# Kernel optimization log

Measured on AMD Instinct MI355X. Metric: run time of the kernel, lower is better.

## Reference

```python
import jax, jax.numpy as jnp
import numpy as np

N = 100000       # nodes
E = 3200000      # edges (avg degree 32)
IN = 64          # in_channels
HID = 32         # hidden_channels
HEADS = 2
OUT = 1
EPS = 1e-5       # LayerNorm eps
SLOPE = 0.2      # LeakyReLU negative slope (PyG default)


def setup_inputs() -> dict:
    key = jax.random.key(0)
    ks = jax.random.split(key, 18)
    def nrm(k, shape, scale=0.1):
        return jax.random.normal(k, shape, dtype=jnp.float32) * scale
    return {
        "x": jax.random.normal(ks[0], (N, IN), dtype=jnp.float32),
        "edge_index": jax.random.randint(ks[1], (2, E), 0, N, dtype=jnp.int64),
        # GATConv layer 1 (concat=True)
        "W1": nrm(ks[2], (IN, HEADS * HID)),
        "a_src1": nrm(ks[3], (HEADS, HID)),
        "a_dst1": nrm(ks[4], (HEADS, HID)),
        "b1": jnp.zeros((HEADS * HID,), jnp.float32),
        "ln1_g": jnp.ones((HEADS * HID,), jnp.float32),
        "ln1_b": jnp.zeros((HEADS * HID,), jnp.float32),
        # GATConv layer 2 (heads=1, concat=False)
        "W2": nrm(ks[5], (HEADS * HID, HID)),
        "a_src2": nrm(ks[6], (1, HID)),
        "a_dst2": nrm(ks[7], (1, HID)),
        "b2": jnp.zeros((HID,), jnp.float32),
        "ln2_g": jnp.ones((HID,), jnp.float32),
        "ln2_b": jnp.zeros((HID,), jnp.float32),
        # output Linear
        "Wout": nrm(ks[8], (HID, OUT)),
        "bout": jnp.zeros((OUT,), jnp.float32),
    }


def layer_norm(x, g, b):
    mu = jnp.mean(x, axis=-1, keepdims=True)
    var = jnp.mean(jnp.square(x - mu), axis=-1, keepdims=True)
    return (x - mu) * jax.lax.rsqrt(var + EPS) * g + b


def gat_conv(x, edge_index, W, a_src, a_dst, bias, heads, ch, concat):
    """PyG GATConv (add_self_loops=True, bias=True), eval mode (no dropout)."""
    n = x.shape[0]
    loop = jnp.arange(n, dtype=edge_index.dtype)
    src = jnp.concatenate([edge_index[0], loop])   # [E+N]
    dst = jnp.concatenate([edge_index[1], loop])   # [E+N]
    h = (x @ W).reshape(n, heads, ch)              # [N,H,C]
    al_src = jnp.sum(h * a_src, axis=-1)           # [N,H]
    al_dst = jnp.sum(h * a_dst, axis=-1)           # [N,H]
    logits = jax.nn.leaky_relu(al_src[src] + al_dst[dst], SLOPE)  # [E+N,H]
    # segment softmax over destination nodes
    m = jax.lax.stop_gradient(jax.ops.segment_max(logits, dst, num_segments=n))
    e = jnp.exp(logits - m[dst])
    denom = jax.ops.segment_sum(e, dst, num_segments=n)
    alpha = e / denom[dst]                         # [E+N,H]
    out = jax.ops.segment_sum(h[src] * alpha[:, :, None], dst, num_segments=n)  # [N,H,C]
    out = out.reshape(n, heads * ch) if concat else out.mean(axis=1)
    return out + bias


def reference(x, edge_index, W1, a_src1, a_dst1, b1, ln1_g, ln1_b,
              W2, a_src2, a_dst2, b2, ln2_g, ln2_b, Wout, bout):
    h = gat_conv(x, edge_index, W1, a_src1, a_dst1, b1, HEADS, HID, True)
    h = jax.nn.elu(layer_norm(h, ln1_g, ln1_b))
    h = gat_conv(h, edge_index, W2, a_src2, a_dst2, b2, 1, HID, False)
    h = jax.nn.elu(layer_norm(h, ln2_g, ln2_b))
    return h @ Wout + bout  # [N, OUT]
```

## Files before the change

kernel.cpp:

```cpp
#include <hip/hip_runtime.h>

#define EPS 1e-5f
#define SLOPE 0.2f
#define MAXK 512
#define SEGCAP 12288
#define PBATCH 16384

__device__ __forceinline__ float leaky(float z) {
    return fmaxf(z, 0.f) + SLOPE * fminf(z, 0.f);
}
__device__ __forceinline__ ushort f2bf(float f) {
    unsigned u = __float_as_uint(f);
    u += 0x7FFFu + ((u >> 16) & 1u);
    return (ushort)(u >> 16);
}
__device__ __forceinline__ float bf2f(ushort b) {
    return __uint_as_float(((unsigned)b) << 16);
}

__global__ __launch_bounds__(256) void hist0(
    const int* __restrict__ ei, int E, int K, int* __restrict__ ghist) {
    __shared__ int h[MAXK];
    int t = threadIdx.x;
    for (int i = t; i < K; i += 256) h[i] = 0;
    __syncthreads();
    int base = blockIdx.x * PBATCH;
    for (int j = 0; j < PBATCH / 256; j++) {
        int e = base + j * 256 + t;
        if (e < E) atomicAdd(&h[ei[E + e] >> 8], 1);
    }
    __syncthreads();
    for (int i = t; i < K; i += 256) if (h[i]) atomicAdd(&ghist[i], h[i]);
}

__global__ __launch_bounds__(512) void scanK(
    const int* __restrict__ ghist, int K, int* __restrict__ segbase,
    int* __restrict__ cursor) {
    __shared__ int sc[512];
    int t = threadIdx.x;
    int v = (t < K) ? ghist[t] : 0;
    sc[t] = v;
    __syncthreads();
    for (int off = 1; off < 512; off <<= 1) {
        int x = (t >= off) ? sc[t - off] : 0;
        __syncthreads();
        sc[t] += x;
        __syncthreads();
    }
    if (t < K) { int ex = sc[t] - v; segbase[t] = ex; cursor[t] = ex; }
    if (t == K - 1) segbase[K] = sc[t];
}

__global__ __launch_bounds__(256) void part1(
    const int* __restrict__ ei, int E, int K, int* __restrict__ cursor,
    unsigned* __restrict__ part) {
    __shared__ int h[MAXK];
    __shared__ int gp[MAXK];
    __shared__ int run[MAXK];
    int t = threadIdx.x;
    for (int i = t; i < K; i += 256) { h[i] = 0; run[i] = 0; }
    __syncthreads();
    int base = blockIdx.x * PBATCH;
    for (int j = 0; j < PBATCH / 256; j++) {
        int e = base + j * 256 + t;
        if (e < E) atomicAdd(&h[ei[E + e] >> 8], 1);
    }
    __syncthreads();
    for (int i = t; i < K; i += 256)
        gp[i] = h[i] ? atomicAdd(&cursor[i], h[i]) : 0;
    __syncthreads();
    for (int j = 0; j < PBATCH / 256; j++) {
        int e = base + j * 256 + t;
        if (e < E) {
            int s = ei[e], d = ei[E + e];
            int b = d >> 8;
            int p = atomicAdd(&run[b], 1);
            part[gp[b] + p] = ((unsigned)s << 8) | (unsigned)(d & 255);
        }
    }
}

__global__ __launch_bounds__(256) void sortseg(
    const int* __restrict__ segbase, int N,
    unsigned* __restrict__ part, int* __restrict__ nodeofs, int* __restrict__ cnt,
    int* __restrict__ perm) {
    __shared__ int h2[2048];
    __shared__ int sc[256];
    __shared__ int ex[256];
    __shared__ unsigned outb[SEGCAP];
    int b = blockIdx.x, t = threadIdx.x;
    int base = segbase[b];
    int sz = segbase[b + 1] - base;
    if (sz > SEGCAP) sz = SEGCAP;
    for (int i = t; i < 2048; i += 256) h2[i] = 0;
    __syncthreads();
    for (int i = t; i < sz; i += 256) {
        unsigned code = part[base + i];
        int key = ((code & 255) << 3) | ((code >> 22) & 7);
        atomicAdd(&h2[key], 1);
    }
    __syncthreads();
    int loc[8];
    int v = 0;
#pragma unroll
    for (int i = 0; i < 8; i++) { loc[i] = h2[t * 8 + i]; v += loc[i]; }
    sc[t] = v;
    __syncthreads();
    for (int off = 1; off < 256; off <<= 1) {
        int x = (t >= off) ? sc[t - off] : 0;
        __syncthreads();
        sc[t] += x;
        __syncthreads();
    }
    int exv = sc[t] - v;
    {
        int run = exv;
#pragma unroll
        for (int i = 0; i < 8; i++) { h2[t * 8 + i] = run; run += loc[i]; }
    }
    int n = b * 256 + t;
    if (n < N) { cnt[n] = v; nodeofs[n] = base + exv; }
    __syncthreads();
    for (int i = t; i < sz; i += 256) {
        unsigned code = part[base + i];
        int key = ((code & 255) << 3) | ((code >> 22) & 7);
        int p = atomicAdd(&h2[key], 1);
        outb[p] = code >> 8;
    }
    __syncthreads();
    for (int i = t; i < sz; i += 256) part[base + i] = outb[i];
    __syncthreads();
    h2[t] = 0;
    __syncthreads();
    int dbin = min(v, 255);
    if (n < N) atomicAdd(&h2[dbin], 1);
    __syncthreads();
    int hv = h2[t];
    sc[t] = hv;
    __syncthreads();
    for (int off = 1; off < 256; off <<= 1) {
        int x = (t >= off) ? sc[t - off] : 0;
        __syncthreads();
        sc[t] += x;
        __syncthreads();
    }
    ex[t] = sc[t] - hv;
    __syncthreads();
    if (n < N) {
        int r = atomicAdd(&ex[dbin], 1);
        perm[b * 256 + r] = n;
    }
}

__global__ __launch_bounds__(256) void prep1(
    const float* __restrict__ x, const float* __restrict__ W1,
    const float* __restrict__ as1, const float* __restrict__ ad1,
    ushort* __restrict__ h1b, float* __restrict__ al_s, float* __restrict__ al_d, int N) {
    __shared__ float Ws[64 * 64];
    __shared__ float xs[16][68];
    int t = threadIdx.x;
    for (int i = t; i < 64 * 64; i += 256) Ws[i] = W1[i];
    int base = blockIdx.x * 16;
    for (int i = t; i < 256; i += 256) {
        int rr = i >> 4, kk = i & 15;
        int gr = base + rr;
        float4 vx = (gr < N) ? ((const float4*)x)[(size_t)gr * 16 + kk]
                             : make_float4(0.f, 0.f, 0.f, 0.f);
        *(float4*)&xs[rr][kk * 4] = vx;
    }
    __syncthreads();
    int wv = t >> 6, c = t & 63;
    int r0 = base + wv * 4;
    float acc0 = 0.f, acc1 = 0.f, acc2 = 0.f, acc3 = 0.f;
#pragma unroll
    for (int k = 0; k < 64; k += 4) {
        float4 x0 = *(const float4*)&xs[wv * 4 + 0][k];
        float4 x1 = *(const float4*)&xs[wv * 4 + 1][k];
        float4 x2 = *(const float4*)&xs[wv * 4 + 2][k];
        float4 x3 = *(const float4*)&xs[wv * 4 + 3][k];
        float w0 = Ws[(k + 0) * 64 + c];
        float w1 = Ws[(k + 1) * 64 + c];
        float w2 = Ws[(k + 2) * 64 + c];
        float w3 = Ws[(k + 3) * 64 + c];
        acc0 = fmaf(x0.x, w0, acc0); acc1 = fmaf(x1.x, w0, acc1);
        acc2 = fmaf(x2.x, w0, acc2); acc3 = fmaf(x3.x, w0, acc3);
        acc0 = fmaf(x0.y, w1, acc0); acc1 = fmaf(x1.y, w1, acc1);
        acc2 = fmaf(x2.y, w1, acc2); acc3 = fmaf(x3.y, w1, acc3);
        acc0 = fmaf(x0.z, w2, acc0); acc1 = fmaf(x1.z, w2, acc1);
        acc2 = fmaf(x2.z, w2, acc2); acc3 = fmaf(x3.z, w2, acc3);
        acc0 = fmaf(x0.w, w3, acc0); acc1 = fmaf(x1.w, w3, acc1);
        acc2 = fmaf(x2.w, w3, acc2); acc3 = fmaf(x3.w, w3, acc3);
    }
    int head = c >> 5, cc = c & 31;
    float asc = as1[head * 32 + cc], adc = ad1[head * 32 + cc];
    float vs0 = acc0 * asc, vd0 = acc0 * adc;
    float vs1 = acc1 * asc, vd1 = acc1 * adc;
    float vs2 = acc2 * asc, vd2 = acc2 * adc;
    float vs3 = acc3 * asc, vd3 = acc3 * adc;
#pragma unroll
    for (int off = 1; off < 32; off <<= 1) {
        vs0 += __shfl_xor(vs0, off); vd0 += __shfl_xor(vd0, off);
        vs1 += __shfl_xor(vs1, off); vd1 += __shfl_xor(vd1, off);
        vs2 += __shfl_xor(vs2, off); vd2 += __shfl_xor(vd2, off);
        vs3 += __shfl_xor(vs3, off); vd3 += __shfl_xor(vd3, off);
    }
    if (r0 + 0 < N) h1b[(size_t)(r0 + 0) * 64 + c] = f2bf(acc0);
    if (r0 + 1 < N) h1b[(size_t)(r0 + 1) * 64 + c] = f2bf(acc1);
    if (r0 + 2 < N) h1b[(size_t)(r0 + 2) * 64 + c] = f2bf(acc2);
    if (r0 + 3 < N) h1b[(size_t)(r0 + 3) * 64 + c] = f2bf(acc3);
    if (cc == 0) {
        if (r0 + 0 < N) { al_s[(r0 + 0) * 2 + head] = vs0; al_d[(r0 + 0) * 2 + head] = vd0; }
        if (r0 + 1 < N) { al_s[(r0 + 1) * 2 + head] = vs1; al_d[(r0 + 1) * 2 + head] = vd1; }
        if (r0 + 2 < N) { al_s[(r0 + 2) * 2 + head] = vs2; al_d[(r0 + 2) * 2 + head] = vd2; }
        if (r0 + 3 < N) { al_s[(r0 + 3) * 2 + head] = vs3; al_d[(r0 + 3) * 2 + head] = vd3; }
    }
}

__global__ __launch_bounds__(256) void aggB1(
    const ushort* __restrict__ h1b, const float* __restrict__ als,
    const float* __restrict__ ald, const int* __restrict__ nodeofs,
    const int* __restrict__ cnt, const unsigned* __restrict__ csr,
    const int* __restrict__ perm,
    const float* __restrict__ b1, const float* __restrict__ g1,
    const float* __restrict__ bb1, ushort* __restrict__ h1out, int N) {
    int lane = threadIdx.x & 63;
    int grp = lane >> 4, q = lane & 15;
    int gbase = grp << 4;
    int idx = blockIdx.x * 16 + (threadIdx.x >> 6) * 4 + grp;
    bool valid = idx < N;
    int nc = perm[min(idx, N - 1)];
    int head = q >> 3;
    const float2* als2 = (const float2*)als;
    const float2* ald2 = (const float2*)ald;
    float2 adv = ald2[nc], asv = als2[nc];
    float ad0 = adv.x, ad1v = adv.y;
    float wsf = __expf(leaky((head ? asv.y : asv.x) + (head ? ad1v : ad0)));
    const ushort4* h4 = (const ushort4*)h1b;
    ushort4 hs = h4[(unsigned)nc * 16 + q];
    float a0 = wsf * bf2f(hs.x), a1 = wsf * bf2f(hs.y);
    float a2 = wsf * bf2f(hs.z), a3 = wsf * bf2f(hs.w);
    float l0p = 0.f, l1p = 0.f;
    int ofs = valid ? nodeofs[nc] : 0;
    int deg = valid ? cnt[nc] : 0;
    int degm1 = max(deg - 1, 0);
    int degmax = deg;
    degmax = max(degmax, __shfl_xor(degmax, 16));
    degmax = max(degmax, __shfl_xor(degmax, 32));
    for (int eb = 0; eb < degmax; eb += 16) {
        int j = ofs + min(eb + q, degm1);
        int sq = min((int)csr[j], N - 1);
        float2 av = als2[sq];
        float z0 = leaky(av.x + ad0);
        float z1 = leaky(av.y + ad1v);
        bool ev = (eb + q < deg);
        float w0q = ev ? __expf(z0) : 0.f;
        float w1q = ev ? __expf(z1) : 0.f;
        l0p += w0q;
        l1p += w1q;
#pragma unroll
        for (int jj = 0; jj < 16; jj++) {
            int s = __shfl(sq, gbase + jj);
            float w0 = __shfl(w0q, gbase + jj);
            float w1 = __shfl(w1q, gbase + jj);
            float w = head ? w1 : w0;
            ushort4 hv = h4[(unsigned)s * 16 + q];
            a0 = fmaf(w, bf2f(hv.x), a0);
            a1 = fmaf(w, bf2f(hv.y), a1);
            a2 = fmaf(w, bf2f(hv.z), a2);
            a3 = fmaf(w, bf2f(hv.w), a3);
        }
    }
#pragma unroll
    for (int off = 1; off < 16; off <<= 1) {
        l0p += __shfl_xor(l0p, off);
        l1p += __shfl_xor(l1p, off);
    }
    if (!valid) return;
    float l = (head ? l1p : l0p) + wsf;
    float inv = 1.f / l;
    float4 bv = ((const float4*)b1)[q];
    float v0 = a0 * inv + bv.x, v1 = a1 * inv + bv.y;
    float v2 = a2 * inv + bv.z, v3 = a3 * inv + bv.w;
    float s1 = v0 + v1 + v2 + v3;
#pragma unroll
    for (int off = 1; off < 16; off <<= 1) s1 += __shfl_xor(s1, off);
    float mu = s1 * (1.f / 64.f);
    float d0 = v0 - mu, d1 = v1 - mu, d2 = v2 - mu, d3 = v3 - mu;
    float s2v = d0 * d0 + d1 * d1 + d2 * d2 + d3 * d3;
#pragma unroll
    for (int off = 1; off < 16; off <<= 1) s2v += __shfl_xor(s2v, off);
    float rs = rsqrtf(s2v * (1.f / 64.f) + EPS);
    float4 gv = ((const float4*)g1)[q];
    float4 bbv = ((const float4*)bb1)[q];
    float y0 = d0 * rs * gv.x + bbv.x;
    float y1 = d1 * rs * gv.y + bbv.y;
    float y2 = d2 * rs * gv.z + bbv.z;
    float y3 = d3 * rs * gv.w + bbv.w;
    y0 = (y0 > 0.f) ? y0 : (__expf(y0) - 1.f);
    y1 = (y1 > 0.f) ? y1 : (__expf(y1) - 1.f);
    y2 = (y2 > 0.f) ? y2 : (__expf(y2) - 1.f);
    y3 = (y3 > 0.f) ? y3 : (__expf(y3) - 1.f);
    ((ushort4*)h1out)[(unsigned)nc * 16 + q] =
        make_ushort4(f2bf(y0), f2bf(y1), f2bf(y2), f2bf(y3));
}

__global__ __launch_bounds__(256) void prep2(
    const ushort* __restrict__ h1ob, const float* __restrict__ W2,
    const float* __restrict__ as2, const float* __restrict__ ad2,
    ushort* __restrict__ h2b, float* __restrict__ al_s, float* __restrict__ al_d, int N) {
    __shared__ float Ws[64 * 32];
    __shared__ float xs[32][68];
    int t = threadIdx.x;
    for (int i = t; i < 64 * 32; i += 256) Ws[i] = W2[i];
    int base = blockIdx.x * 32;
    const ushort4* hv4 = (const ushort4*)h1ob;
    for (int i = t; i < 512; i += 256) {
        int rr = i >> 4, kk = i & 15;
        int gr = base + rr;
        ushort4 u = (gr < N) ? hv4[(unsigned)gr * 16 + kk] : make_ushort4(0, 0, 0, 0);
        xs[rr][kk * 4 + 0] = bf2f(u.x);
        xs[rr][kk * 4 + 1] = bf2f(u.y);
        xs[rr][kk * 4 + 2] = bf2f(u.z);
        xs[rr][kk * 4 + 3] = bf2f(u.w);
    }
    __syncthreads();
    int wv = t >> 6;
    int lane = t & 63;
    int half = lane >> 5, c = lane & 31;
    int rbase = wv * 8 + half * 4;
    int r0 = base + rbase;
    float acc0 = 0.f, acc1 = 0.f, acc2 = 0.f, acc3 = 0.f;
#pragma unroll
    for (int k = 0; k < 64; k += 4) {
        float4 x0 = *(const float4*)&xs[rbase + 0][k];
        float4 x1 = *(const float4*)&xs[rbase + 1][k];
        float4 x2 = *(const float4*)&xs[rbase + 2][k];
        float4 x3 = *(const float4*)&xs[rbase + 3][k];
        float w0 = Ws[(k + 0) * 32 + c];
        float w1 = Ws[(k + 1) * 32 + c];
        float w2 = Ws[(k + 2) * 32 + c];
        float w3 = Ws[(k + 3) * 32 + c];
        acc0 = fmaf(x0.x, w0, acc0); acc1 = fmaf(x1.x, w0, acc1);
        acc2 = fmaf(x2.x, w0, acc2); acc3 = fmaf(x3.x, w0, acc3);
        acc0 = fmaf(x0.y, w1, acc0); acc1 = fmaf(x1.y, w1, acc1);
        acc2 = fmaf(x2.y, w1, acc2); acc3 = fmaf(x3.y, w1, acc3);
        acc0 = fmaf(x0.z, w2, acc0); acc1 = fmaf(x1.z, w2, acc1);
        acc2 = fmaf(x2.z, w2, acc2); acc3 = fmaf(x3.z, w2, acc3);
        acc0 = fmaf(x0.w, w3, acc0); acc1 = fmaf(x1.w, w3, acc1);
        acc2 = fmaf(x2.w, w3, acc2); acc3 = fmaf(x3.w, w3, acc3);
    }
    float asc = as2[c], adc = ad2[c];
    float vs0 = acc0 * asc, vd0 = acc0 * adc;
    float vs1 = acc1 * asc, vd1 = acc1 * adc;
    float vs2 = acc2 * asc, vd2 = acc2 * adc;
    float vs3 = acc3 * asc, vd3 = acc3 * adc;
#pragma unroll
    for (int off = 1; off < 32; off <<= 1) {
        vs0 += __shfl_xor(vs0, off); vd0 += __shfl_xor(vd0, off);
        vs1 += __shfl_xor(vs1, off); vd1 += __shfl_xor(vd1, off);
        vs2 += __shfl_xor(vs2, off); vd2 += __shfl_xor(vd2, off);
        vs3 += __shfl_xor(vs3, off); vd3 += __shfl_xor(vd3, off);
    }
    if (r0 + 0 < N) h2b[(size_t)(r0 + 0) * 32 + c] = f2bf(acc0);
    if (r0 + 1 < N) h2b[(size_t)(r0 + 1) * 32 + c] = f2bf(acc1);
    if (r0 + 2 < N) h2b[(size_t)(r0 + 2) * 32 + c] = f2bf(acc2);
    if (r0 + 3 < N) h2b[(size_t)(r0 + 3) * 32 + c] = f2bf(acc3);
    if (c == 0) {
        if (r0 + 0 < N) { al_s[r0 + 0] = vs0; al_d[r0 + 0] = vd0; }
        if (r0 + 1 < N) { al_s[r0 + 1] = vs1; al_d[r0 + 1] = vd1; }
        if (r0 + 2 < N) { al_s[r0 + 2] = vs2; al_d[r0 + 2] = vd2; }
        if (r0 + 3 < N) { al_s[r0 + 3] = vs3; al_d[r0 + 3] = vd3; }
    }
}

__global__ __launch_bounds__(256) void aggB2(
    const ushort* __restrict__ h2b, const float* __restrict__ als,
    const float* __restrict__ ald, const int* __restrict__ nodeofs,
    const int* __restrict__ cnt, const unsigned* __restrict__ csr,
    const int* __restrict__ perm,
    const float* __restrict__ b2, const float* __restrict__ g2,
    const float* __restrict__ bb2, const float* __restrict__ Wout,
    const float* __restrict__ bout, float* __restrict__ out, int N) {
    int lane = threadIdx.x & 63;
    int grp = lane >> 3, q = lane & 7;
    int gbase = grp << 3;
    int idx = blockIdx.x * 32 + (threadIdx.x >> 6) * 8 + grp;
    bool valid = idx < N;
    int nc = perm[min(idx, N - 1)];
    float myad = ald[nc];
    float wsf = __expf(leaky(als[nc] + myad));
    const ushort4* h4 = (const ushort4*)h2b;
    ushort4 hs = h4[(unsigned)nc * 8 + q];
    float a0 = wsf * bf2f(hs.x), a1 = wsf * bf2f(hs.y);
    float a2 = wsf * bf2f(hs.z), a3 = wsf * bf2f(hs.w);
    float lp = 0.f;
    int ofs = valid ? nodeofs[nc] : 0;
    int deg = valid ? cnt[nc] : 0;
    int degm1 = max(deg - 1, 0);
    int degmax = deg;
    degmax = max(degmax, __shfl_xor(degmax, 8));
    degmax = max(degmax, __shfl_xor(degmax, 16));
    degmax = max(degmax, __shfl_xor(degmax, 32));
    for (int eb = 0; eb < degmax; eb += 8) {
        int j = ofs + min(eb + q, degm1);
        int sq = min((int)csr[j], N - 1);
        float z = leaky(als[sq] + myad);
        float wq = (eb + q < deg) ? __expf(z) : 0.f;
        lp += wq;
#pragma unroll
        for (int jj = 0; jj < 8; jj++) {
            int s = __shfl(sq, gbase + jj);
            float w = __shfl(wq, gbase + jj);
            ushort4 hv = h4[(unsigned)s * 8 + q];
            a0 = fmaf(w, bf2f(hv.x), a0);
            a1 = fmaf(w, bf2f(hv.y), a1);
            a2 = fmaf(w, bf2f(hv.z), a2);
            a3 = fmaf(w, bf2f(hv.w), a3);
        }
    }
#pragma unroll
    for (int off = 1; off < 8; off <<= 1) lp += __shfl_xor(lp, off);
    if (!valid) return;
    float l = lp + wsf;
    float inv = 1.f / l;
    float4 bv = ((const float4*)b2)[q];
    float v0 = a0 * inv + bv.x, v1 = a1 * inv + bv.y;
    float v2 = a2 * inv + bv.z, v3 = a3 * inv + bv.w;
    float s1 = v0 + v1 + v2 + v3;
#pragma unroll
    for (int off = 1; off < 8; off <<= 1) s1 += __shfl_xor(s1, off);
    float mu = s1 * (1.f / 32.f);
    float d0 = v0 - mu, d1 = v1 - mu, d2 = v2 - mu, d3 = v3 - mu;
    float s2v = d0 * d0 + d1 * d1 + d2 * d2 + d3 * d3;
#pragma unroll
    for (int off = 1; off < 8; off <<= 1) s2v += __shfl_xor(s2v, off);
    float rs = rsqrtf(s2v * (1.f / 32.f) + EPS);
    float4 gv = ((const float4*)g2)[q];
    float4 bbv = ((const float4*)bb2)[q];
    float y0 = d0 * rs * gv.x + bbv.x;
    float y1 = d1 * rs * gv.y + bbv.y;
    float y2 = d2 * rs * gv.z + bbv.z;
    float y3 = d3 * rs * gv.w + bbv.w;
    y0 = (y0 > 0.f) ? y0 : (__expf(y0) - 1.f);
    y1 = (y1 > 0.f) ? y1 : (__expf(y1) - 1.f);
    y2 = (y2 > 0.f) ? y2 : (__expf(y2) - 1.f);
    y3 = (y3 > 0.f) ? y3 : (__expf(y3) - 1.f);
    float4 wo = ((const float4*)Wout)[q];
    float p = y0 * wo.x + y1 * wo.y + y2 * wo.z + y3 * wo.w;
#pragma unroll
    for (int off = 1; off < 8; off <<= 1) p += __shfl_xor(p, off);
    if (q == 0) out[nc] = p + bout[0];
}

extern "C" void kernel_launch(void* const* d_in, const int* in_sizes, int n_in,
                              void* d_out, int out_size, void* d_ws, size_t ws_size,
                              hipStream_t stream) {
    const float* x    = (const float*)d_in[0];
    const int*   ei   = (const int*)d_in[1];
    const float* W1   = (const float*)d_in[2];
    const float* as1  = (const float*)d_in[3];
    const float* ad1  = (const float*)d_in[4];
    const float* b1   = (const float*)d_in[5];
    const float* g1   = (const float*)d_in[6];
    const float* bb1  = (const float*)d_in[7];
    const float* W2   = (const float*)d_in[8];
    const float* as2  = (const float*)d_in[9];
    const float* ad2  = (const float*)d_in[10];
    const float* b2   = (const float*)d_in[11];
    const float* g2   = (const float*)d_in[12];
    const float* bb2  = (const float*)d_in[13];
    const float* Wout = (const float*)d_in[14];
    const float* bout = (const float*)d_in[15];
    float* out = (float*)d_out;

    const int N = in_sizes[0] / 64;
    const int E = in_sizes[1] / 2;
    const int K = (N + 255) / 256;

    auto align_up = [](size_t v) { return (v + 255) & ~(size_t)255; };
    char* ws = (char*)d_ws;
    unsigned* part    = (unsigned*)ws; ws += align_up((size_t)E * 4);
    int*      nodeofs = (int*)ws;      ws += align_up((size_t)N * 4);
    int*      cnt     = (int*)ws;      ws += align_up((size_t)N * 4);
    int*      perm    = (int*)ws;      ws += align_up((size_t)(K * 256) * 4);
    int*      ghist   = (int*)ws;      ws += align_up((size_t)(MAXK) * 4);
    int*      segbase = (int*)ws;      ws += align_up((size_t)(MAXK + 1) * 4);
    int*      cursor  = (int*)ws;      ws += align_up((size_t)(MAXK) * 4);
    ushort*   h1b     = (ushort*)ws;   ws += align_up((size_t)N * 64 * 2);
    ushort*   h1ob    = (ushort*)ws;   ws += align_up((size_t)N * 64 * 2);
    ushort*   h2b     = (ushort*)ws;   ws += align_up((size_t)N * 32 * 2);
    float*    al1s    = (float*)ws;    ws += align_up((size_t)N * 2 * 4);
    float*    al1d    = (float*)ws;    ws += align_up((size_t)N * 2 * 4);
    float*    al2s    = (float*)ws;    ws += align_up((size_t)N * 4);
    float*    al2d    = (float*)ws;    ws += align_up((size_t)N * 4);

    const int EB = (E + PBATCH - 1) / PBATCH;

    hipMemsetAsync(ghist, 0, (size_t)K * 4, stream);
    hist0<<<EB, 256, 0, stream>>>(ei, E, K, ghist);
    scanK<<<1, 512, 0, stream>>>(ghist, K, segbase, cursor);
    part1<<<EB, 256, 0, stream>>>(ei, E, K, cursor, part);
    sortseg<<<K, 256, 0, stream>>>(segbase, N, part, nodeofs, cnt, perm);

    prep1<<<(N + 15) / 16, 256, 0, stream>>>(x, W1, as1, ad1, h1b, al1s, al1d, N);
    aggB1<<<(N + 15) / 16, 256, 0, stream>>>(h1b, al1s, al1d, nodeofs, cnt, part,
                                             perm, b1, g1, bb1, h1ob, N);
    prep2<<<(N + 31) / 32, 256, 0, stream>>>(h1ob, W2, as2, ad2, h2b, al2s, al2d, N);
    aggB2<<<(N + 31) / 32, 256, 0, stream>>>(h2b, al2s, al2d, nodeofs, cnt, part,
                                             perm, b2, g2, bb2, Wout, bout, out, N);
}
```

Before: 363.8 us.

## Use fixed-capacity segments to drop histogram pass and pad CSR rows for vector loads

Replaces the global histogram and scan kernels with fixed-capacity per-segment buckets (SEGCAP each), so the edge partition runs as one pass that uses atomic counters per segment. sortseg now pads each node's adjacency list to a multiple of 4 with zeros and sorts on a finer key. The aggregation kernels read neighbor indices with int4 vector loads instead of broadcasting them through shuffles. In layer 1 the two head weights are packed into one bf16 pair so each edge needs a single shuffle. This removes two kernel launches and a full read of the edge list, and cuts shuffle traffic. In exchange, the partition buffer is larger, bf16 rounding is applied to the attention weights, and edges beyond SEGCAP in a segment are silently dropped. The int4 loads can also read past the padded row into the next node's entries, which is only safe because their weights are zero.

```diff
diff --git a/kernel.cpp b/kernel.cpp
--- a/kernel.cpp
+++ b/kernel.cpp
@@ -18,41 +18,8 @@
     return __uint_as_float(((unsigned)b) << 16);
 }
 
-__global__ __launch_bounds__(256) void hist0(
-    const int* __restrict__ ei, int E, int K, int* __restrict__ ghist) {
-    __shared__ int h[MAXK];
-    int t = threadIdx.x;
-    for (int i = t; i < K; i += 256) h[i] = 0;
-    __syncthreads();
-    int base = blockIdx.x * PBATCH;
-    for (int j = 0; j < PBATCH / 256; j++) {
-        int e = base + j * 256 + t;
-        if (e < E) atomicAdd(&h[ei[E + e] >> 8], 1);
-    }
-    __syncthreads();
-    for (int i = t; i < K; i += 256) if (h[i]) atomicAdd(&ghist[i], h[i]);
-}
-
-__global__ __launch_bounds__(512) void scanK(
-    const int* __restrict__ ghist, int K, int* __restrict__ segbase,
-    int* __restrict__ cursor) {
-    __shared__ int sc[512];
-    int t = threadIdx.x;
-    int v = (t < K) ? ghist[t] : 0;
-    sc[t] = v;
-    __syncthreads();
-    for (int off = 1; off < 512; off <<= 1) {
-        int x = (t >= off) ? sc[t - off] : 0;
-        __syncthreads();
-        sc[t] += x;
-        __syncthreads();
-    }
-    if (t < K) { int ex = sc[t] - v; segbase[t] = ex; cursor[t] = ex; }
-    if (t == K - 1) segbase[K] = sc[t];
-}
-
 __global__ __launch_bounds__(256) void part1(
-    const int* __restrict__ ei, int E, int K, int* __restrict__ cursor,
+    const int* __restrict__ ei, int E, int K, int* __restrict__ segcnt,
     unsigned* __restrict__ part) {
     __shared__ int h[MAXK];
     __shared__ int gp[MAXK];
@@ -67,44 +34,45 @@
     }
     __syncthreads();
     for (int i = t; i < K; i += 256)
-        gp[i] = h[i] ? atomicAdd(&cursor[i], h[i]) : 0;
+        gp[i] = h[i] ? atomicAdd(&segcnt[i], h[i]) : 0;
     __syncthreads();
     for (int j = 0; j < PBATCH / 256; j++) {
         int e = base + j * 256 + t;
         if (e < E) {
             int s = ei[e], d = ei[E + e];
             int b = d >> 8;
-            int p = atomicAdd(&run[b], 1);
-            part[gp[b] + p] = ((unsigned)s << 8) | (unsigned)(d & 255);
+            int p = atomicAdd(&run[b], 1) + gp[b];
+            if (p < SEGCAP)
+                part[(size_t)b * SEGCAP + p] = ((unsigned)s << 8) | (unsigned)(d & 255);
         }
     }
 }
 
 __global__ __launch_bounds__(256) void sortseg(
-    const int* __restrict__ segbase, int N,
+    const int* __restrict__ segcnt, int N,
     unsigned* __restrict__ part, int* __restrict__ nodeofs, int* __restrict__ cnt,
     int* __restrict__ perm) {
-    __shared__ int h2[2048];
+    __shared__ int h2[4096];
     __shared__ int sc[256];
     __shared__ int ex[256];
     __shared__ unsigned outb[SEGCAP];
     int b = blockIdx.x, t = threadIdx.x;
-    int base = segbase[b];
-    int sz = segbase[b + 1] - base;
-    if (sz > SEGCAP) sz = SEGCAP;
-    for (int i = t; i < 2048; i += 256) h2[i] = 0;
+    size_t base = (size_t)b * SEGCAP;
+    int sz = min(segcnt[b], SEGCAP);
+    for (int i = t; i < 4096; i += 256) h2[i] = 0;
     __syncthreads();
     for (int i = t; i < sz; i += 256) {
         unsigned code = part[base + i];
-        int key = ((code & 255) << 3) | ((code >> 22) & 7);
+        int key = ((code & 255) << 4) | ((code >> 21) & 15);
         atomicAdd(&h2[key], 1);
     }
     __syncthreads();
-    int loc[8];
+    int loc[16];
     int v = 0;
 #pragma unroll
-    for (int i = 0; i < 8; i++) { loc[i] = h2[t * 8 + i]; v += loc[i]; }
-    sc[t] = v;
+    for (int i = 0; i < 16; i++) { loc[i] = h2[t * 16 + i]; v += loc[i]; }
+    int vp = (v + 3) & ~3;
+    sc[t] = vp;
     __syncthreads();
     for (int off = 1; off < 256; off <<= 1) {
         int x = (t >= off) ? sc[t - off] : 0;
@@ -112,23 +80,26 @@
         sc[t] += x;
         __syncthreads();
     }
-    int exv = sc[t] - v;
+    int exv = sc[t] - vp;
     {
         int run = exv;
 #pragma unroll
-        for (int i = 0; i < 8; i++) { h2[t * 8 + i] = run; run += loc[i]; }
+        for (int i = 0; i < 16; i++) { h2[t * 16 + i] = run; run += loc[i]; }
     }
     int n = b * 256 + t;
-    if (n < N) { cnt[n] = v; nodeofs[n] = base + exv; }
+    if (n < N) { cnt[n] = v; nodeofs[n] = (int)(base + exv); }
+    int szp = sc[255];
+    __syncthreads();
+    for (int i = t; i < szp; i += 256) outb[i] = 0;
     __syncthreads();
     for (int i = t; i < sz; i += 256) {
         unsigned code = part[base + i];
-        int key = ((code & 255) << 3) | ((code >> 22) & 7);
+        int key = ((code & 255) << 4) | ((code >> 21) & 15);
         int p = atomicAdd(&h2[key], 1);
         outb[p] = code >> 8;
     }
     __syncthreads();
-    for (int i = t; i < sz; i += 256) part[base + i] = outb[i];
+    for (int i = t; i < szp; i += 256) part[base + i] = outb[i];
     __syncthreads();
     h2[t] = 0;
     __syncthreads();
@@ -230,6 +201,7 @@
     bool valid = idx < N;
     int nc = perm[min(idx, N - 1)];
     int head = q >> 3;
+    int hshift = head << 4;
     const float2* als2 = (const float2*)als;
     const float2* ald2 = (const float2*)ald;
     float2 adv = ald2[nc], asv = als2[nc];
@@ -246,9 +218,10 @@
     int degmax = deg;
     degmax = max(degmax, __shfl_xor(degmax, 16));
     degmax = max(degmax, __shfl_xor(degmax, 32));
+    unsigned nm1 = (unsigned)(N - 1);
     for (int eb = 0; eb < degmax; eb += 16) {
         int j = ofs + min(eb + q, degm1);
-        int sq = min((int)csr[j], N - 1);
+        int sq = (int)min((unsigned)csr[j], nm1);
         float2 av = als2[sq];
         float z0 = leaky(av.x + ad0);
         float z1 = leaky(av.y + ad1v);
@@ -257,12 +230,16 @@
         float w1q = ev ? __expf(z1) : 0.f;
         l0p += w0q;
         l1p += w1q;
+        unsigned wp = ((unsigned)f2bf(w1q) << 16) | f2bf(w0q);
+        const int4* c4 = (const int4*)(csr + ofs + eb);
+        int4 ca = c4[0], cb = c4[1], cc4 = c4[2], cd = c4[3];
+        int ss[16] = {ca.x, ca.y, ca.z, ca.w, cb.x, cb.y, cb.z, cb.w,
+                      cc4.x, cc4.y, cc4.z, cc4.w, cd.x, cd.y, cd.z, cd.w};
 #pragma unroll
         for (int jj = 0; jj < 16; jj++) {
-            int s = __shfl(sq, gbase + jj);
-            float w0 = __shfl(w0q, gbase + jj);
-            float w1 = __shfl(w1q, gbase + jj);
-            float w = head ? w1 : w0;
+            int s = (int)min((unsigned)ss[jj], nm1);
+            unsigned wpj = (unsigned)__shfl((int)wp, gbase + jj);
+            float w = bf2f((ushort)((wpj >> hshift) & 0xFFFFu));
             ushort4 hv = h4[(unsigned)s * 16 + q];
             a0 = fmaf(w, bf2f(hv.x), a0);
             a1 = fmaf(w, bf2f(hv.y), a1);
@@ -401,15 +378,19 @@
     degmax = max(degmax, __shfl_xor(degmax, 8));
     degmax = max(degmax, __shfl_xor(degmax, 16));
     degmax = max(degmax, __shfl_xor(degmax, 32));
+    unsigned nm1 = (unsigned)(N - 1);
     for (int eb = 0; eb < degmax; eb += 8) {
         int j = ofs + min(eb + q, degm1);
-        int sq = min((int)csr[j], N - 1);
+        int sq = (int)min((unsigned)csr[j], nm1);
         float z = leaky(als[sq] + myad);
         float wq = (eb + q < deg) ? __expf(z) : 0.f;
         lp += wq;
+        const int4* c4 = (const int4*)(csr + ofs + eb);
+        int4 ca = c4[0], cb = c4[1];
+        int ss[8] = {ca.x, ca.y, ca.z, ca.w, cb.x, cb.y, cb.z, cb.w};
 #pragma unroll
         for (int jj = 0; jj < 8; jj++) {
-            int s = __shfl(sq, gbase + jj);
+            int s = (int)min((unsigned)ss[jj], nm1);
             float w = __shfl(wq, gbase + jj);
             ushort4 hv = h4[(unsigned)s * 8 + q];
             a0 = fmaf(w, bf2f(hv.x), a0);
@@ -479,13 +460,11 @@
 
     auto align_up = [](size_t v) { return (v + 255) & ~(size_t)255; };
     char* ws = (char*)d_ws;
-    unsigned* part    = (unsigned*)ws; ws += align_up((size_t)E * 4);
+    unsigned* part    = (unsigned*)ws; ws += align_up((size_t)K * SEGCAP * 4);
+    int*      segcnt  = (int*)ws;      ws += align_up((size_t)MAXK * 4);
     int*      nodeofs = (int*)ws;      ws += align_up((size_t)N * 4);
     int*      cnt     = (int*)ws;      ws += align_up((size_t)N * 4);
     int*      perm    = (int*)ws;      ws += align_up((size_t)(K * 256) * 4);
-    int*      ghist   = (int*)ws;      ws += align_up((size_t)(MAXK) * 4);
-    int*      segbase = (int*)ws;      ws += align_up((size_t)(MAXK + 1) * 4);
-    int*      cursor  = (int*)ws;      ws += align_up((size_t)(MAXK) * 4);
     ushort*   h1b     = (ushort*)ws;   ws += align_up((size_t)N * 64 * 2);
     ushort*   h1ob    = (ushort*)ws;   ws += align_up((size_t)N * 64 * 2);
     ushort*   h2b     = (ushort*)ws;   ws += align_up((size_t)N * 32 * 2);
@@ -496,11 +475,9 @@
 
     const int EB = (E + PBATCH - 1) / PBATCH;
 
-    hipMemsetAsync(ghist, 0, (size_t)K * 4, stream);
-    hist0<<<EB, 256, 0, stream>>>(ei, E, K, ghist);
-    scanK<<<1, 512, 0, stream>>>(ghist, K, segbase, cursor);
-    part1<<<EB, 256, 0, stream>>>(ei, E, K, cursor, part);
-    sortseg<<<K, 256, 0, stream>>>(segbase, N, part, nodeofs, cnt, perm);
+    hipMemsetAsync(segcnt, 0, (size_t)K * 4, stream);
+    part1<<<EB, 256, 0, stream>>>(ei, E, K, segcnt, part);
+    sortseg<<<K, 256, 0, stream>>>(segcnt, N, part, nodeofs, cnt, perm);
 
     prep1<<<(N + 15) / 16, 256, 0, stream>>>(x, W1, as1, ad1, h1b, al1s, al1d, N);
     aggB1<<<(N + 15) / 16, 256, 0, stream>>>(h1b, al1s, al1d, nodeofs, cnt, part,
```

Measured after the change: 384.5 us. +5.7%, slower.
